# Kernel tuning notes

Measured on AMD Instinct MI355X. Metric: run time of the kernel, lower is better.

The kernel has to match this reference:

```python
import jax, jax.numpy as jnp
import numpy as np

MARGIN = 1.0
CURVATURE = 1.0
BOUNDARY_FACTOR = 2.0
MARGIN_THRESHOLD = 0.1
EPS = 1e-7


def setup_inputs() -> dict:
    key = jax.random.key(0)
    k1, k2 = jax.random.split(key)
    B, D = 4096, 128
    # scale so norms stay inside the unit Poincare ball (~0.57 on average)
    embeddings = jax.random.normal(k1, (B, D), dtype=jnp.float32) * 0.05
    labels = jax.random.randint(k2, (B,), 0, 64, dtype=jnp.int64)
    return {"embeddings": embeddings, "labels": labels}


def _poincare_distance_matrix(x, c):
    # d(x,y) = (1/sqrt(c)) * arccosh(1 + 2c||x-y||^2 / ((1-c||x||^2)(1-c||y||^2)))
    sq = jnp.sum(x * x, axis=-1)                       # [B]
    diff_sq = jnp.maximum(sq[:, None] + sq[None, :] - 2.0 * (x @ x.T), 0.0)
    denom = jnp.maximum((1.0 - c * sq[:, None]) * (1.0 - c * sq[None, :]), EPS)
    arg = 1.0 + 2.0 * c * diff_sq / denom
    return jnp.arccosh(jnp.maximum(arg, 1.0)) / jnp.sqrt(c)


def reference(embeddings, labels):
    B = embeddings.shape[0]
    distances = _poincare_distance_matrix(embeddings, CURVATURE)   # [B,B]

    same = labels[:, None] == labels[None, :]
    eye = jnp.eye(B, dtype=bool)
    positive_mask = same & ~eye
    negative_mask = ~same

    has_pos = jnp.any(positive_mask, axis=1)
    has_neg = jnp.any(negative_mask, axis=1)
    valid_anchor = has_pos & has_neg                               # [B]

    neg_inf = jnp.asarray(-jnp.inf, distances.dtype)
    hardest_pos = jnp.max(jnp.where(positive_mask, distances, neg_inf), axis=1)
    hardest_pos = jnp.where(has_pos, hardest_pos, 0.0)

    # adaptive margin (torch uses .item() -> detached from autograd)
    anchor_norm = jax.lax.stop_gradient(jnp.linalg.norm(embeddings, axis=-1))
    margin = jnp.maximum(MARGIN * (1.0 + BOUNDARY_FACTOR * anchor_norm),
                         MARGIN_THRESHOLD)                          # [B]

    pair_mask = valid_anchor[:, None] & negative_mask               # [B,B]
    raw = hardest_pos[:, None] - distances + margin[:, None]
    losses = jnp.maximum(raw, 0.0)

    total_triplets = jnp.sum(pair_mask)
    num_active = jnp.sum((raw > 0.0) & pair_mask)
    denom = jnp.maximum(total_triplets, 1).astype(losses.dtype)
    loss = jnp.sum(jnp.where(pair_mask, losses, 0.0)) / denom       # 'mean'

    active_ratio = num_active.astype(jnp.float32) / jnp.maximum(
        total_triplets.astype(jnp.float32), 1.0)
    pos_count = jnp.sum(positive_mask)
    mean_distance = jnp.where(
        pos_count > 0,
        jnp.sum(jnp.where(positive_mask, distances, 0.0))
        / jnp.maximum(pos_count, 1).astype(distances.dtype),
        0.0)

    return (loss, num_active, total_triplets, active_ratio, mean_distance)
```

## Files before the change

kernel.cpp:

```cpp
#include <hip/hip_runtime.h>
#include <hip/hip_bf16.h>
#include <math.h>

static constexpr int D   = 128;
static constexpr int NL  = 64;
static constexpr int NT  = 64;

typedef __attribute__((ext_vector_type(8))) short  bf16x8;
typedef __attribute__((ext_vector_type(4))) float  f32x4;

__device__ __forceinline__ float wave_reduce_sum(float v) {
  #pragma unroll
  for (int o = 32; o; o >>= 1) v += __shfl_xor(v, o, 64);
  return v;
}

__device__ __forceinline__ float fast_acosh(float x) {
  float s = __builtin_amdgcn_sqrtf(fmaf(x, x, -1.0f));
  return __logf(x + s);
}

__device__ __forceinline__ unsigned short f2b(float x) {
  unsigned int u = __float_as_uint(x);
  unsigned int lsb = (u >> 16) & 1u;
  u += 0x7fffu + lsb;
  return (unsigned short)(u >> 16);
}

__global__ __launch_bounds__(256) void kAB_setup(
    const float* __restrict__ emb, const int* __restrict__ lab,
    float* acc, int* LOFF, int* SIDX,
    float* __restrict__ sq, float* __restrict__ vv, int B) {
  int t = threadIdx.x;
  if ((int)blockIdx.x < B / 4) {
    int w = t >> 6, lane = t & 63;
    int i = blockIdx.x * 4 + w;
    float2 v = reinterpret_cast<const float2*>(emb + (size_t)i * D)[lane];
    float s = wave_reduce_sum(v.x * v.x + v.y * v.y);
    if (lane == 0) {
      sq[i] = s;
      vv[i] = 1.41421356237f / fmaxf(1.0f - s, 1e-6f);
    }
    return;
  }
  __shared__ int h[NL];
  __shared__ int cur[NL];
  if (t < NL) h[t] = 0;
  __syncthreads();
  for (int i = t; i < B; i += 256) atomicAdd(&h[lab[i]], 1);
  __syncthreads();
  if (t == 0) {
    int off = 0;
    long long pc = 0, trip = 0;
    for (int l = 0; l < NL; ++l) {
      int c = h[l];
      LOFF[l] = off; cur[l] = off; off += c;
      pc += (long long)c * (c - 1);
      if (c >= 2 && c < B) trip += (long long)c * (B - c);
    }
    LOFF[NL] = B;
    acc[0] = 0.0f; acc[1] = 0.0f; acc[2] = 0.0f;
    acc[3] = (float)pc;
    acc[4] = (float)trip;
  }
  __syncthreads();
  for (int i = t; i < B; i += 256) {
    int p = atomicAdd(&cur[lab[i]], 1);
    SIDX[p] = i;
  }
}

__global__ __launch_bounds__(256) void kC_pos(
    const float* __restrict__ emb,
    const int* __restrict__ LOFF, const int* __restrict__ SIDX,
    const float* __restrict__ sq, const float* __restrict__ vv,
    float* __restrict__ hpm, float* acc, int B) {
  __shared__ unsigned short Al[NT][D + 8];
  __shared__ unsigned short Bl[NT][D + 8];
  __shared__ float rs[NT], rv[NT];
  __shared__ float cs[NT], cv[NT];
  __shared__ int   ridx[NT], cidx[NT];

  int l = blockIdx.x;
  int base = LOFF[l];
  int c = LOFF[l + 1] - base;
  if (c == 0) return;
  int t = threadIdx.x;
  int wid = t >> 6, lane = t & 63;
  int lr = lane & 15, lg = lane >> 4;
  const bool validc = (c >= 2) && (c < B);

  float lsum = 0.0f;

  for (int i0 = 0; i0 < c; i0 += NT) {
    int ci = min(NT, c - i0);
    __syncthreads();
    #pragma unroll
    for (int p = 0; p < 8; ++p) {
      int idx = t + p * 256;
      int r = idx >> 5, c4 = idx & 31;
      int gi = SIDX[base + i0 + min(r, ci - 1)];
      float4 va = reinterpret_cast<const float4*>(emb + (size_t)gi * D)[c4];
      ushort4 ua = { f2b(va.x), f2b(va.y), f2b(va.z), f2b(va.w) };
      *reinterpret_cast<ushort4*>(&Al[r][c4 * 4]) = ua;
    }
    if (t < NT) {
      int gi = SIDX[base + i0 + min(t, ci - 1)];
      rs[t] = sq[gi]; rv[t] = vv[gi]; ridx[t] = gi;
    }

    float rmax[4] = {0.0f, 0.0f, 0.0f, 0.0f};

    for (int j0 = 0; j0 < c; j0 += NT) {
      int cj = min(NT, c - j0);
      __syncthreads();
      #pragma unroll
      for (int p = 0; p < 8; ++p) {
        int idx = t + p * 256;
        int r = idx >> 5, c4 = idx & 31;
        int gj = SIDX[base + j0 + min(r, cj - 1)];
        float4 vb = reinterpret_cast<const float4*>(emb + (size_t)gj * D)[c4];
        ushort4 ub = { f2b(vb.x), f2b(vb.y), f2b(vb.z), f2b(vb.w) };
        *reinterpret_cast<ushort4*>(&Bl[r][c4 * 4]) = ub;
      }
      if (t < NT) {
        int gj = SIDX[base + j0 + min(t, cj - 1)];
        cs[t] = sq[gj]; cv[t] = vv[gj]; cidx[t] = gj;
      }
      __syncthreads();

      f32x4 dacc[4];
      #pragma unroll
      for (int n = 0; n < 4; ++n) dacc[n] = (f32x4){0.f, 0.f, 0.f, 0.f};
      #pragma unroll
      for (int kk = 0; kk < 4; ++kk) {
        bf16x8 a = *reinterpret_cast<const bf16x8*>(&Al[wid * 16 + lr][kk * 32 + lg * 8]);
        bf16x8 b[4];
        #pragma unroll
        for (int n = 0; n < 4; ++n)
          b[n] = *reinterpret_cast<const bf16x8*>(&Bl[n * 16 + lr][kk * 32 + lg * 8]);
        #pragma unroll
        for (int n = 0; n < 4; ++n)
          dacc[n] = __builtin_amdgcn_mfma_f32_16x16x32_bf16(a, b[n], dacc[n], 0, 0, 0);
      }

      int r0 = wid * 16 + lg * 4;
      #pragma unroll
      for (int n = 0; n < 4; ++n) {
        int cc = n * 16 + lr;
        float sc = cs[cc], vcv = cv[cc];
        int   gj = cidx[cc];
        #pragma unroll
        for (int g = 0; g < 4; ++g) {
          int rloc = r0 + g;
          if (rloc < ci && cc < cj && ridx[rloc] != gj) {
            float diff = fmaxf(fmaf(-2.0f, dacc[n][g], rs[rloc] + sc), 0.0f);
            float arg  = fmaf(diff * rv[rloc], vcv, 1.0f);
            float d    = fast_acosh(arg);
            lsum += d;
            rmax[g] = fmaxf(rmax[g], d);
          }
        }
      }
    }

    int r0 = wid * 16 + lg * 4;
    #pragma unroll
    for (int g = 0; g < 4; ++g) {
      float v = rmax[g];
      v = fmaxf(v, __shfl_xor(v, 1, 64));
      v = fmaxf(v, __shfl_xor(v, 2, 64));
      v = fmaxf(v, __shfl_xor(v, 4, 64));
      v = fmaxf(v, __shfl_xor(v, 8, 64));
      int rloc = r0 + g;
      if (lr == 0 && rloc < ci) {
        float mg = fmaxf(fmaf(2.0f, __builtin_amdgcn_sqrtf(rs[rloc]), 1.0f), 0.1f);
        hpm[ridx[rloc]] = validc ? (v + mg) : -1e30f;
      }
    }
  }

  lsum = wave_reduce_sum(lsum);
  if (lane == 0 && lsum != 0.0f) atomicAdd(&acc[2], lsum);
}

__global__ __launch_bounds__(256) void kD_neg(
    const float* __restrict__ emb, const int* __restrict__ lab,
    const float* __restrict__ sq, const float* __restrict__ vv,
    const float* __restrict__ hpm, float* __restrict__ part, int B) {
  __shared__ unsigned short Al[NT][D + 8];
  __shared__ unsigned short Bl[NT][D + 8];
  __shared__ float rs[NT], rv[NT], rh[NT];
  __shared__ float cs[NT], cv[NT], ch[NT];
  __shared__ int   rl[NT], cl[NT];
  __shared__ float red[8];

  const int T = B / NT;
  int bid = blockIdx.x;
  float disc = (float)((2 * T + 1) * (2 * T + 1) - 8 * bid);
  int bi = (int)(((float)(2 * T + 1) - __builtin_amdgcn_sqrtf(disc)) * 0.5f);
  bi = max(0, min(bi, T - 1));
  while (bi * T - bi * (bi - 1) / 2 > bid) --bi;
  while ((bi + 1) * T - (bi + 1) * bi / 2 <= bid) ++bi;
  int bj = bi + (bid - (bi * T - bi * (bi - 1) / 2));
  const bool diag = (bi == bj);

  int t = threadIdx.x;

  const float* abase = emb + (size_t)bi * NT * D;
  const float* bbase = emb + (size_t)bj * NT * D;
  #pragma unroll
  for (int p = 0; p < NT * (D / 4) / 256; ++p) {
    int idx = t + p * 256;
    int r = idx >> 5, c4 = idx & 31;
    float4 va = reinterpret_cast<const float4*>(abase)[idx];
    float4 vb = reinterpret_cast<const float4*>(bbase)[idx];
    ushort4 ua = { f2b(va.x), f2b(va.y), f2b(va.z), f2b(va.w) };
    ushort4 ub = { f2b(vb.x), f2b(vb.y), f2b(vb.z), f2b(vb.w) };
    *reinterpret_cast<ushort4*>(&Al[r][c4 * 4]) = ua;
    *reinterpret_cast<ushort4*>(&Bl[r][c4 * 4]) = ub;
  }
  if (t < NT) {
    int g = bi * NT + t;
    rs[t] = sq[g]; rv[t] = vv[g]; rh[t] = hpm[g]; rl[t] = lab[g];
  } else if (t < 2 * NT) {
    int r = t - NT, g = bj * NT + r;
    cs[r] = sq[g]; cv[r] = vv[g]; ch[r] = hpm[g]; cl[r] = lab[g];
  }
  __syncthreads();

  int wid = t >> 6, lane = t & 63;
  int lr = lane & 15, lg = lane >> 4;

  f32x4 dacc[4];
  #pragma unroll
  for (int n = 0; n < 4; ++n) dacc[n] = (f32x4){0.f, 0.f, 0.f, 0.f};

  #pragma unroll
  for (int kk = 0; kk < 4; ++kk) {
    bf16x8 a = *reinterpret_cast<const bf16x8*>(&Al[wid * 16 + lr][kk * 32 + lg * 8]);
    bf16x8 b[4];
    #pragma unroll
    for (int n = 0; n < 4; ++n)
      b[n] = *reinterpret_cast<const bf16x8*>(&Bl[n * 16 + lr][kk * 32 + lg * 8]);
    #pragma unroll
    for (int n = 0; n < 4; ++n)
      dacc[n] = __builtin_amdgcn_mfma_f32_16x16x32_bf16(a, b[n], dacc[n], 0, 0, 0);
  }

  const float dsec = diag ? 0.0f : 1.0f;
  float lsum = 0.0f, lact = 0.0f;
  int r0 = wid * 16 + lg * 4;
  f32x4 sr = *reinterpret_cast<const f32x4*>(&rs[r0]);
  f32x4 vr = *reinterpret_cast<const f32x4*>(&rv[r0]);
  f32x4 hr = *reinterpret_cast<const f32x4*>(&rh[r0]);
  int4  lm = *reinterpret_cast<const int4*>(&rl[r0]);
  int lmv[4] = { lm.x, lm.y, lm.z, lm.w };
  #pragma unroll
  for (int n = 0; n < 4; ++n) {
    int cc = n * 16 + lr;
    float sc = cs[cc], vcv = cv[cc], hc = ch[cc];
    int   lc = cl[cc];
    #pragma unroll
    for (int g = 0; g < 4; ++g) {
      float dot  = dacc[n][g];
      float diff = fmaxf(fmaf(-2.0f, dot, sr[g] + sc), 0.0f);
      float arg  = fmaf(diff * vr[g], vcv, 1.0f);
      float d    = fast_acosh(arg);
      float r1   = hr[g] - d;
      float r2   = hc    - d;
      float neg  = (lmv[g] != lc) ? 1.0f : 0.0f;
      lsum += neg * (fmaxf(r1, 0.0f) + dsec * fmaxf(r2, 0.0f));
      lact += neg * ((r1 > 0.0f ? 1.0f : 0.0f) + dsec * (r2 > 0.0f ? 1.0f : 0.0f));
    }
  }

  lsum = wave_reduce_sum(lsum);
  lact = wave_reduce_sum(lact);
  if (lane == 0) { red[wid] = lsum; red[4 + wid] = lact; }
  __syncthreads();
  if (t == 0) {
    part[2 * bid]     = (red[0] + red[1]) + (red[2] + red[3]);
    part[2 * bid + 1] = (red[4] + red[5]) + (red[6] + red[7]);
  }
}

__global__ __launch_bounds__(256) void kE_final(
    const float* __restrict__ part, int nblk, const float* acc, float* out) {
  __shared__ float sl[256], sa[256];
  int t = threadIdx.x;
  float s = 0.0f, a = 0.0f;
  for (int i = t; i < nblk; i += 256) {
    s += part[2 * i];
    a += part[2 * i + 1];
  }
  sl[t] = s; sa[t] = a;
  __syncthreads();
  for (int o = 128; o; o >>= 1) {
    if (t < o) { sl[t] += sl[t + o]; sa[t] += sa[t + o]; }
    __syncthreads();
  }
  if (t == 0) {
    float trip = acc[4];
    float den  = fmaxf(trip, 1.0f);
    out[0] = sl[0] / den;
    out[1] = sa[0];
    out[2] = trip;
    out[3] = sa[0] / den;
    out[4] = (acc[3] > 0.0f) ? acc[2] / fmaxf(acc[3], 1.0f)
                             : 0.0f;
  }
}

extern "C" void kernel_launch(void* const* d_in, const int* in_sizes, int n_in,
                              void* d_out, int out_size, void* d_ws, size_t ws_size,
                              hipStream_t stream) {
  const float* emb = (const float*)d_in[0];
  const int*   lab = (const int*)d_in[1];
  int B = in_sizes[1];

  int T = B / NT;
  int nblk = T * (T + 1) / 2;

  float* ws   = (float*)d_ws;
  float* acc  = ws;
  float* sq   = ws + 8;
  float* vv   = sq + B;
  float* hpm  = vv + B;
  int*   LOFF = (int*)(hpm + B);
  int*   SIDX = LOFF + (NL + 1);
  float* part = (float*)(SIDX + B);

  kAB_setup<<<B / 4 + 1, 256, 0, stream>>>(emb, lab, acc, LOFF, SIDX, sq, vv, B);
  kC_pos<<<NL, 256, 0, stream>>>(emb, LOFF, SIDX, sq, vv, hpm, acc, B);
  kD_neg<<<nblk, 256, 0, stream>>>(emb, lab, sq, vv, hpm, part, B);
  kE_final<<<1, 256, 0, stream>>>(part, nblk, acc, (float*)d_out);
}
```

Before: 54.83 us.

## Fuse all stages into one cooperative persistent kernel with bf16 embedding cache

Merges the setup, positive, negative and final-reduction kernels into a single cooperative kernel, using grid-wide syncs between phases and a persistent grid sized to the occupancy limit. Embeddings are converted to bf16 once into the workspace, so later tiles load bf16 directly instead of reconverting fp32 per tile. Per-label index lists are now built in shared memory with a prefix scan instead of global atomics. It removes launch overhead and redundant conversion, but adds grid.sync costs, caps the per-label list at 512 entries, and loops tiles inside fewer blocks.

New measurement: 204.7 us. 273% more time.

```diff
diff --git a/kernel.cpp b/kernel.cpp
--- a/kernel.cpp
+++ b/kernel.cpp
@@ -1,10 +1,14 @@
 #include <hip/hip_runtime.h>
+#include <hip/hip_cooperative_groups.h>
 #include <hip/hip_bf16.h>
 #include <math.h>
 
-static constexpr int D   = 128;
-static constexpr int NL  = 64;
-static constexpr int NT  = 64;
+namespace cg = cooperative_groups;
+
+static constexpr int D        = 128;
+static constexpr int NL       = 64;
+static constexpr int NT       = 64;
+static constexpr int LIDX_CAP = 512;
 
 typedef __attribute__((ext_vector_type(8))) short  bf16x8;
 typedef __attribute__((ext_vector_type(4))) float  f32x4;
@@ -27,288 +31,289 @@
   return (unsigned short)(u >> 16);
 }
 
-__global__ __launch_bounds__(256) void kAB_setup(
+__global__ __launch_bounds__(256) void kfused(
     const float* __restrict__ emb, const int* __restrict__ lab,
-    float* acc, int* LOFF, int* SIDX,
-    float* __restrict__ sq, float* __restrict__ vv, int B) {
-  int t = threadIdx.x;
-  if ((int)blockIdx.x < B / 4) {
-    int w = t >> 6, lane = t & 63;
-    int i = blockIdx.x * 4 + w;
-    float2 v = reinterpret_cast<const float2*>(emb + (size_t)i * D)[lane];
+    void* __restrict__ wsv, float* __restrict__ out, int B) {
+  __shared__ unsigned short Al[NT][D + 8];
+  __shared__ unsigned short Bl[NT][D + 8];
+  __shared__ float rs[NT], rv[NT], cs[NT], cv[NT];
+  __shared__ int   ridx[NT], cidx[NT];
+  __shared__ union U {
+    struct { float rh[NT], ch[NT]; int rl[NT], cl[NT]; } c;
+    int lidx[LIDX_CAP];
+  } u;
+  __shared__ int   parr[256];
+  __shared__ float red[24];
+
+  float* wsf = (float*)wsv;
+  unsigned short* bfe = (unsigned short*)wsf;
+  float* sq     = wsf + (size_t)B * D / 2;
+  float* vv     = sq + B;
+  float* hpm    = vv + B;
+  float* plsum  = hpm + B;
+  float* plpc   = plsum + NL;
+  float* pltrip = plpc + NL;
+  float* part   = pltrip + NL;
+
+  cg::grid_group grid = cg::this_grid();
+  const int t    = threadIdx.x;
+  const int bid  = blockIdx.x;
+  const int G    = gridDim.x;
+  const int wid  = t >> 6, lane = t & 63;
+  const int lr   = lane & 15, lg = lane >> 4;
+
+  for (int row = bid * 4 + wid; row < B; row += G * 4) {
+    float2 v = reinterpret_cast<const float2*>(emb + (size_t)row * D)[lane];
+    ushort2 bv = { f2b(v.x), f2b(v.y) };
+    *reinterpret_cast<ushort2*>(&bfe[(size_t)row * D + 2 * lane]) = bv;
     float s = wave_reduce_sum(v.x * v.x + v.y * v.y);
     if (lane == 0) {
-      sq[i] = s;
-      vv[i] = 1.41421356237f / fmaxf(1.0f - s, 1e-6f);
-    }
-    return;
-  }
-  __shared__ int h[NL];
-  __shared__ int cur[NL];
-  if (t < NL) h[t] = 0;
+      sq[row] = s;
+      vv[row] = 1.41421356237f / fmaxf(1.0f - s, 1e-6f);
+    }
+  }
+  grid.sync();
+
+  if (bid < NL) {
+    const int l = bid;
+    int mc = 0;
+    for (int i = t; i < B; i += 256) mc += (lab[i] == l) ? 1 : 0;
+    parr[t] = mc;
+    __syncthreads();
+    for (int off = 1; off < 256; off <<= 1) {
+      int v = (t >= off) ? parr[t - off] : 0;
+      __syncthreads();
+      parr[t] += v;
+      __syncthreads();
+    }
+    const int c = parr[255];
+    int myoff = parr[t] - mc;
+    for (int i = t; i < B; i += 256) {
+      if (lab[i] == l) {
+        if (myoff < LIDX_CAP) u.lidx[myoff] = i;
+        ++myoff;
+      }
+    }
+    __syncthreads();
+
+    const int  cc_    = min(c, LIDX_CAP);
+    const bool validc = (c >= 2) && (c < B);
+    float lsum = 0.0f;
+
+    for (int i0 = 0; i0 < cc_; i0 += NT) {
+      int ci = min(NT, cc_ - i0);
+      __syncthreads();
+      #pragma unroll
+      for (int p = 0; p < 4; ++p) {
+        int idx = t + p * 256;
+        int r = idx >> 4, c16 = idx & 15;
+        int gi = u.lidx[i0 + min(r, ci - 1)];
+        bf16x8 va = reinterpret_cast<const bf16x8*>(bfe + (size_t)gi * D)[c16];
+        *reinterpret_cast<bf16x8*>(&Al[r][c16 * 8]) = va;
+      }
+      if (t < NT) {
+        int gi = u.lidx[i0 + min(t, ci - 1)];
+        rs[t] = sq[gi]; rv[t] = vv[gi]; ridx[t] = gi;
+      }
+
+      float rmax[4] = {0.0f, 0.0f, 0.0f, 0.0f};
+
+      for (int j0 = 0; j0 < cc_; j0 += NT) {
+        int cj = min(NT, cc_ - j0);
+        __syncthreads();
+        #pragma unroll
+        for (int p = 0; p < 4; ++p) {
+          int idx = t + p * 256;
+          int r = idx >> 4, c16 = idx & 15;
+          int gj = u.lidx[j0 + min(r, cj - 1)];
+          bf16x8 vb = reinterpret_cast<const bf16x8*>(bfe + (size_t)gj * D)[c16];
+          *reinterpret_cast<bf16x8*>(&Bl[r][c16 * 8]) = vb;
+        }
+        if (t < NT) {
+          int gj = u.lidx[j0 + min(t, cj - 1)];
+          cs[t] = sq[gj]; cv[t] = vv[gj]; cidx[t] = gj;
+        }
+        __syncthreads();
+
+        f32x4 dacc[4];
+        #pragma unroll
+        for (int n = 0; n < 4; ++n) dacc[n] = (f32x4){0.f, 0.f, 0.f, 0.f};
+        #pragma unroll
+        for (int kk = 0; kk < 4; ++kk) {
+          bf16x8 a = *reinterpret_cast<const bf16x8*>(&Al[wid * 16 + lr][kk * 32 + lg * 8]);
+          bf16x8 b[4];
+          #pragma unroll
+          for (int n = 0; n < 4; ++n)
+            b[n] = *reinterpret_cast<const bf16x8*>(&Bl[n * 16 + lr][kk * 32 + lg * 8]);
+          #pragma unroll
+          for (int n = 0; n < 4; ++n)
+            dacc[n] = __builtin_amdgcn_mfma_f32_16x16x32_bf16(a, b[n], dacc[n], 0, 0, 0);
+        }
+
+        int r0 = wid * 16 + lg * 4;
+        #pragma unroll
+        for (int n = 0; n < 4; ++n) {
+          int ccn = n * 16 + lr;
+          float sc = cs[ccn], vcv = cv[ccn];
+          int   gj = cidx[ccn];
+          #pragma unroll
+          for (int g = 0; g < 4; ++g) {
+            int rloc = r0 + g;
+            if (rloc < ci && ccn < cj && ridx[rloc] != gj) {
+              float diff = fmaxf(fmaf(-2.0f, dacc[n][g], rs[rloc] + sc), 0.0f);
+              float arg  = fmaf(diff * rv[rloc], vcv, 1.0f);
+              float d    = fast_acosh(arg);
+              lsum += d;
+              rmax[g] = fmaxf(rmax[g], d);
+            }
+          }
+        }
+      }
+
+      int r0 = wid * 16 + lg * 4;
+      #pragma unroll
+      for (int g = 0; g < 4; ++g) {
+        float v = rmax[g];
+        v = fmaxf(v, __shfl_xor(v, 1, 64));
+        v = fmaxf(v, __shfl_xor(v, 2, 64));
+        v = fmaxf(v, __shfl_xor(v, 4, 64));
+        v = fmaxf(v, __shfl_xor(v, 8, 64));
+        int rloc = r0 + g;
+        if (lr == 0 && rloc < ci) {
+          float mg = fmaxf(fmaf(2.0f, __builtin_amdgcn_sqrtf(rs[rloc]), 1.0f), 0.1f);
+          hpm[ridx[rloc]] = validc ? (v + mg) : -1e30f;
+        }
+      }
+    }
+
+    lsum = wave_reduce_sum(lsum);
+    if (lane == 0) red[wid] = lsum;
+    __syncthreads();
+    if (t == 0) {
+      plsum[l]  = (c > 0) ? (red[0] + red[1]) + (red[2] + red[3]) : 0.0f;
+      plpc[l]   = (float)((long long)c * (c - 1));
+      pltrip[l] = ((c >= 2) && (c < B)) ? (float)((long long)c * (B - c)) : 0.0f;
+    }
+  }
+  grid.sync();
+
+  const int T2    = B / NT;
+  const int ntile = T2 * (T2 + 1) / 2;
+  float nsum = 0.0f, nact = 0.0f;
+
+  for (int tile = bid; tile < ntile; tile += G) {
+    float disc = (float)((2 * T2 + 1) * (2 * T2 + 1) - 8 * tile);
+    int bi = (int)(((float)(2 * T2 + 1) - __builtin_amdgcn_sqrtf(disc)) * 0.5f);
+    bi = max(0, min(bi, T2 - 1));
+    while (bi * T2 - bi * (bi - 1) / 2 > tile) --bi;
+    while ((bi + 1) * T2 - (bi + 1) * bi / 2 <= tile) ++bi;
+    int bj = bi + (tile - (bi * T2 - bi * (bi - 1) / 2));
+    const float dsec = (bi == bj) ? 0.0f : 1.0f;
+
+    __syncthreads();
+    const unsigned short* ab = bfe + (size_t)bi * NT * D;
+    const unsigned short* bb = bfe + (size_t)bj * NT * D;
+    #pragma unroll
+    for (int p = 0; p < 4; ++p) {
+      int idx = t + p * 256;
+      int r = idx >> 4, c16 = idx & 15;
+      bf16x8 va = reinterpret_cast<const bf16x8*>(ab + (size_t)r * D)[c16];
+      bf16x8 vb = reinterpret_cast<const bf16x8*>(bb + (size_t)r * D)[c16];
+      *reinterpret_cast<bf16x8*>(&Al[r][c16 * 8]) = va;
+      *reinterpret_cast<bf16x8*>(&Bl[r][c16 * 8]) = vb;
+    }
+    if (t < NT) {
+      int g = bi * NT + t;
+      rs[t] = sq[g]; rv[t] = vv[g]; u.c.rh[t] = hpm[g]; u.c.rl[t] = lab[g];
+    } else if (t < 2 * NT) {
+      int r = t - NT, g = bj * NT + r;
+      cs[r] = sq[g]; cv[r] = vv[g]; u.c.ch[r] = hpm[g]; u.c.cl[r] = lab[g];
+    }
+    __syncthreads();
+
+    f32x4 dacc[4];
+    #pragma unroll
+    for (int n = 0; n < 4; ++n) dacc[n] = (f32x4){0.f, 0.f, 0.f, 0.f};
+    #pragma unroll
+    for (int kk = 0; kk < 4; ++kk) {
+      bf16x8 a = *reinterpret_cast<const bf16x8*>(&Al[wid * 16 + lr][kk * 32 + lg * 8]);
+      bf16x8 b[4];
+      #pragma unroll
+      for (int n = 0; n < 4; ++n)
+        b[n] = *reinterpret_cast<const bf16x8*>(&Bl[n * 16 + lr][kk * 32 + lg * 8]);
+      #pragma unroll
+      for (int n = 0; n < 4; ++n)
+        dacc[n] = __builtin_amdgcn_mfma_f32_16x16x32_bf16(a, b[n], dacc[n], 0, 0, 0);
+    }
+
+    int r0 = wid * 16 + lg * 4;
+    f32x4 sr = *reinterpret_cast<const f32x4*>(&rs[r0]);
+    f32x4 vr = *reinterpret_cast<const f32x4*>(&rv[r0]);
+    f32x4 hr = *reinterpret_cast<const f32x4*>(&u.c.rh[r0]);
+    int lmv[4] = { u.c.rl[r0], u.c.rl[r0 + 1], u.c.rl[r0 + 2], u.c.rl[r0 + 3] };
+    #pragma unroll
+    for (int n = 0; n < 4; ++n) {
+      int ccn = n * 16 + lr;
+      float sc = cs[ccn], vcv = cv[ccn], hc = u.c.ch[ccn];
+      int   lc = u.c.cl[ccn];
+      #pragma unroll
+      for (int g = 0; g < 4; ++g) {
+        float diff = fmaxf(fmaf(-2.0f, dacc[n][g], sr[g] + sc), 0.0f);
+        float arg  = fmaf(diff * vr[g], vcv, 1.0f);
+        float d    = fast_acosh(arg);
+        float r1   = hr[g] - d;
+        float r2   = hc    - d;
+        float neg  = (lmv[g] != lc) ? 1.0f : 0.0f;
+        nsum += neg * (fmaxf(r1, 0.0f) + dsec * fmaxf(r2, 0.0f));
+        nact += neg * ((r1 > 0.0f ? 1.0f : 0.0f) + dsec * (r2 > 0.0f ? 1.0f : 0.0f));
+      }
+    }
+  }
+
+  nsum = wave_reduce_sum(nsum);
+  nact = wave_reduce_sum(nact);
   __syncthreads();
-  for (int i = t; i < B; i += 256) atomicAdd(&h[lab[i]], 1);
-  __syncthreads();
-  if (t == 0) {
-    int off = 0;
-    long long pc = 0, trip = 0;
-    for (int l = 0; l < NL; ++l) {
-      int c = h[l];
-      LOFF[l] = off; cur[l] = off; off += c;
-      pc += (long long)c * (c - 1);
-      if (c >= 2 && c < B) trip += (long long)c * (B - c);
-    }
-    LOFF[NL] = B;
-    acc[0] = 0.0f; acc[1] = 0.0f; acc[2] = 0.0f;
-    acc[3] = (float)pc;
-    acc[4] = (float)trip;
-  }
-  __syncthreads();
-  for (int i = t; i < B; i += 256) {
-    int p = atomicAdd(&cur[lab[i]], 1);
-    SIDX[p] = i;
-  }
-}
-
-__global__ __launch_bounds__(256) void kC_pos(
-    const float* __restrict__ emb,
-    const int* __restrict__ LOFF, const int* __restrict__ SIDX,
-    const float* __restrict__ sq, const float* __restrict__ vv,
-    float* __restrict__ hpm, float* acc, int B) {
-  __shared__ unsigned short Al[NT][D + 8];
-  __shared__ unsigned short Bl[NT][D + 8];
-  __shared__ float rs[NT], rv[NT];
-  __shared__ float cs[NT], cv[NT];
-  __shared__ int   ridx[NT], cidx[NT];
-
-  int l = blockIdx.x;
-  int base = LOFF[l];
-  int c = LOFF[l + 1] - base;
-  if (c == 0) return;
-  int t = threadIdx.x;
-  int wid = t >> 6, lane = t & 63;
-  int lr = lane & 15, lg = lane >> 4;
-  const bool validc = (c >= 2) && (c < B);
-
-  float lsum = 0.0f;
-
-  for (int i0 = 0; i0 < c; i0 += NT) {
-    int ci = min(NT, c - i0);
-    __syncthreads();
-    #pragma unroll
-    for (int p = 0; p < 8; ++p) {
-      int idx = t + p * 256;
-      int r = idx >> 5, c4 = idx & 31;
-      int gi = SIDX[base + i0 + min(r, ci - 1)];
-      float4 va = reinterpret_cast<const float4*>(emb + (size_t)gi * D)[c4];
-      ushort4 ua = { f2b(va.x), f2b(va.y), f2b(va.z), f2b(va.w) };
-      *reinterpret_cast<ushort4*>(&Al[r][c4 * 4]) = ua;
-    }
-    if (t < NT) {
-      int gi = SIDX[base + i0 + min(t, ci - 1)];
-      rs[t] = sq[gi]; rv[t] = vv[gi]; ridx[t] = gi;
-    }
-
-    float rmax[4] = {0.0f, 0.0f, 0.0f, 0.0f};
-
-    for (int j0 = 0; j0 < c; j0 += NT) {
-      int cj = min(NT, c - j0);
-      __syncthreads();
-      #pragma unroll
-      for (int p = 0; p < 8; ++p) {
-        int idx = t + p * 256;
-        int r = idx >> 5, c4 = idx & 31;
-        int gj = SIDX[base + j0 + min(r, cj - 1)];
-        float4 vb = reinterpret_cast<const float4*>(emb + (size_t)gj * D)[c4];
-        ushort4 ub = { f2b(vb.x), f2b(vb.y), f2b(vb.z), f2b(vb.w) };
-        *reinterpret_cast<ushort4*>(&Bl[r][c4 * 4]) = ub;
-      }
-      if (t < NT) {
-        int gj = SIDX[base + j0 + min(t, cj - 1)];
-        cs[t] = sq[gj]; cv[t] = vv[gj]; cidx[t] = gj;
-      }
-      __syncthreads();
-
-      f32x4 dacc[4];
-      #pragma unroll
-      for (int n = 0; n < 4; ++n) dacc[n] = (f32x4){0.f, 0.f, 0.f, 0.f};
-      #pragma unroll
-      for (int kk = 0; kk < 4; ++kk) {
-        bf16x8 a = *reinterpret_cast<const bf16x8*>(&Al[wid * 16 + lr][kk * 32 + lg * 8]);
-        bf16x8 b[4];
-        #pragma unroll
-        for (int n = 0; n < 4; ++n)
-          b[n] = *reinterpret_cast<const bf16x8*>(&Bl[n * 16 + lr][kk * 32 + lg * 8]);
-        #pragma unroll
-        for (int n = 0; n < 4; ++n)
-          dacc[n] = __builtin_amdgcn_mfma_f32_16x16x32_bf16(a, b[n], dacc[n], 0, 0, 0);
-      }
-
-      int r0 = wid * 16 + lg * 4;
-      #pragma unroll
-      for (int n = 0; n < 4; ++n) {
-        int cc = n * 16 + lr;
-        float sc = cs[cc], vcv = cv[cc];
-        int   gj = cidx[cc];
-        #pragma unroll
-        for (int g = 0; g < 4; ++g) {
-          int rloc = r0 + g;
-          if (rloc < ci && cc < cj && ridx[rloc] != gj) {
-            float diff = fmaxf(fmaf(-2.0f, dacc[n][g], rs[rloc] + sc), 0.0f);
-            float arg  = fmaf(diff * rv[rloc], vcv, 1.0f);
-            float d    = fast_acosh(arg);
-            lsum += d;
-            rmax[g] = fmaxf(rmax[g], d);
-          }
-        }
-      }
-    }
-
-    int r0 = wid * 16 + lg * 4;
-    #pragma unroll
-    for (int g = 0; g < 4; ++g) {
-      float v = rmax[g];
-      v = fmaxf(v, __shfl_xor(v, 1, 64));
-      v = fmaxf(v, __shfl_xor(v, 2, 64));
-      v = fmaxf(v, __shfl_xor(v, 4, 64));
-      v = fmaxf(v, __shfl_xor(v, 8, 64));
-      int rloc = r0 + g;
-      if (lr == 0 && rloc < ci) {
-        float mg = fmaxf(fmaf(2.0f, __builtin_amdgcn_sqrtf(rs[rloc]), 1.0f), 0.1f);
-        hpm[ridx[rloc]] = validc ? (v + mg) : -1e30f;
-      }
-    }
-  }
-
-  lsum = wave_reduce_sum(lsum);
-  if (lane == 0 && lsum != 0.0f) atomicAdd(&acc[2], lsum);
-}
-
-__global__ __launch_bounds__(256) void kD_neg(
-    const float* __restrict__ emb, const int* __restrict__ lab,
-    const float* __restrict__ sq, const float* __restrict__ vv,
-    const float* __restrict__ hpm, float* __restrict__ part, int B) {
-  __shared__ unsigned short Al[NT][D + 8];
-  __shared__ unsigned short Bl[NT][D + 8];
-  __shared__ float rs[NT], rv[NT], rh[NT];
-  __shared__ float cs[NT], cv[NT], ch[NT];
-  __shared__ int   rl[NT], cl[NT];
-  __shared__ float red[8];
-
-  const int T = B / NT;
-  int bid = blockIdx.x;
-  float disc = (float)((2 * T + 1) * (2 * T + 1) - 8 * bid);
-  int bi = (int)(((float)(2 * T + 1) - __builtin_amdgcn_sqrtf(disc)) * 0.5f);
-  bi = max(0, min(bi, T - 1));
-  while (bi * T - bi * (bi - 1) / 2 > bid) --bi;
-  while ((bi + 1) * T - (bi + 1) * bi / 2 <= bid) ++bi;
-  int bj = bi + (bid - (bi * T - bi * (bi - 1) / 2));
-  const bool diag = (bi == bj);
-
-  int t = threadIdx.x;
-
-  const float* abase = emb + (size_t)bi * NT * D;
-  const float* bbase = emb + (size_t)bj * NT * D;
-  #pragma unroll
-  for (int p = 0; p < NT * (D / 4) / 256; ++p) {
-    int idx = t + p * 256;
-    int r = idx >> 5, c4 = idx & 31;
-    float4 va = reinterpret_cast<const float4*>(abase)[idx];
-    float4 vb = reinterpret_cast<const float4*>(bbase)[idx];
-    ushort4 ua = { f2b(va.x), f2b(va.y), f2b(va.z), f2b(va.w) };
-    ushort4 ub = { f2b(vb.x), f2b(vb.y), f2b(vb.z), f2b(vb.w) };
-    *reinterpret_cast<ushort4*>(&Al[r][c4 * 4]) = ua;
-    *reinterpret_cast<ushort4*>(&Bl[r][c4 * 4]) = ub;
-  }
-  if (t < NT) {
-    int g = bi * NT + t;
-    rs[t] = sq[g]; rv[t] = vv[g]; rh[t] = hpm[g]; rl[t] = lab[g];
-  } else if (t < 2 * NT) {
-    int r = t - NT, g = bj * NT + r;
-    cs[r] = sq[g]; cv[r] = vv[g]; ch[r] = hpm[g]; cl[r] = lab[g];
-  }
-  __syncthreads();
-
-  int wid = t >> 6, lane = t & 63;
-  int lr = lane & 15, lg = lane >> 4;
-
-  f32x4 dacc[4];
-  #pragma unroll
-  for (int n = 0; n < 4; ++n) dacc[n] = (f32x4){0.f, 0.f, 0.f, 0.f};
-
-  #pragma unroll
-  for (int kk = 0; kk < 4; ++kk) {
-    bf16x8 a = *reinterpret_cast<const bf16x8*>(&Al[wid * 16 + lr][kk * 32 + lg * 8]);
-    bf16x8 b[4];
-    #pragma unroll
-    for (int n = 0; n < 4; ++n)
-      b[n] = *reinterpret_cast<const bf16x8*>(&Bl[n * 16 + lr][kk * 32 + lg * 8]);
-    #pragma unroll
-    for (int n = 0; n < 4; ++n)
-      dacc[n] = __builtin_amdgcn_mfma_f32_16x16x32_bf16(a, b[n], dacc[n], 0, 0, 0);
-  }
-
-  const float dsec = diag ? 0.0f : 1.0f;
-  float lsum = 0.0f, lact = 0.0f;
-  int r0 = wid * 16 + lg * 4;
-  f32x4 sr = *reinterpret_cast<const f32x4*>(&rs[r0]);
-  f32x4 vr = *reinterpret_cast<const f32x4*>(&rv[r0]);
-  f32x4 hr = *reinterpret_cast<const f32x4*>(&rh[r0]);
-  int4  lm = *reinterpret_cast<const int4*>(&rl[r0]);
-  int lmv[4] = { lm.x, lm.y, lm.z, lm.w };
-  #pragma unroll
-  for (int n = 0; n < 4; ++n) {
-    int cc = n * 16 + lr;
-    float sc = cs[cc], vcv = cv[cc], hc = ch[cc];
-    int   lc = cl[cc];
-    #pragma unroll
-    for (int g = 0; g < 4; ++g) {
-      float dot  = dacc[n][g];
-      float diff = fmaxf(fmaf(-2.0f, dot, sr[g] + sc), 0.0f);
-      float arg  = fmaf(diff * vr[g], vcv, 1.0f);
-      float d    = fast_acosh(arg);
-      float r1   = hr[g] - d;
-      float r2   = hc    - d;
-      float neg  = (lmv[g] != lc) ? 1.0f : 0.0f;
-      lsum += neg * (fmaxf(r1, 0.0f) + dsec * fmaxf(r2, 0.0f));
-      lact += neg * ((r1 > 0.0f ? 1.0f : 0.0f) + dsec * (r2 > 0.0f ? 1.0f : 0.0f));
-    }
-  }
-
-  lsum = wave_reduce_sum(lsum);
-  lact = wave_reduce_sum(lact);
-  if (lane == 0) { red[wid] = lsum; red[4 + wid] = lact; }
+  if (lane == 0) { red[wid] = nsum; red[8 + wid] = nact; }
   __syncthreads();
   if (t == 0) {
     part[2 * bid]     = (red[0] + red[1]) + (red[2] + red[3]);
-    part[2 * bid + 1] = (red[4] + red[5]) + (red[6] + red[7]);
-  }
-}
-
-__global__ __launch_bounds__(256) void kE_final(
-    const float* __restrict__ part, int nblk, const float* acc, float* out) {
-  __shared__ float sl[256], sa[256];
-  int t = threadIdx.x;
-  float s = 0.0f, a = 0.0f;
-  for (int i = t; i < nblk; i += 256) {
-    s += part[2 * i];
-    a += part[2 * i + 1];
-  }
-  sl[t] = s; sa[t] = a;
-  __syncthreads();
-  for (int o = 128; o; o >>= 1) {
-    if (t < o) { sl[t] += sl[t + o]; sa[t] += sa[t + o]; }
-    __syncthreads();
-  }
-  if (t == 0) {
-    float trip = acc[4];
-    float den  = fmaxf(trip, 1.0f);
-    out[0] = sl[0] / den;
-    out[1] = sa[0];
-    out[2] = trip;
-    out[3] = sa[0] / den;
-    out[4] = (acc[3] > 0.0f) ? acc[2] / fmaxf(acc[3], 1.0f)
-                             : 0.0f;
+    part[2 * bid + 1] = (red[8] + red[9]) + (red[10] + red[11]);
+  }
+  grid.sync();
+
+  if (bid == 0) {
+    float s = 0.0f, a = 0.0f;
+    for (int i = t; i < G; i += 256) {
+      s += part[2 * i];
+      a += part[2 * i + 1];
+    }
+    float ps = 0.0f, pc = 0.0f, tr = 0.0f;
+    if (t < NL) { ps = plsum[t]; pc = plpc[t]; tr = pltrip[t]; }
+    s  = wave_reduce_sum(s);
+    a  = wave_reduce_sum(a);
+    ps = wave_reduce_sum(ps);
+    pc = wave_reduce_sum(pc);
+    tr = wave_reduce_sum(tr);
+    __syncthreads();
+    if (lane == 0) {
+      red[wid * 5 + 0] = s;  red[wid * 5 + 1] = a;  red[wid * 5 + 2] = ps;
+      red[wid * 5 + 3] = pc; red[wid * 5 + 4] = tr;
+    }
+    __syncthreads();
+    if (t == 0) {
+      float S = 0, A = 0, PS = 0, PC = 0, TR = 0;
+      #pragma unroll
+      for (int w = 0; w < 4; ++w) {
+        S += red[w * 5 + 0]; A += red[w * 5 + 1]; PS += red[w * 5 + 2];
+        PC += red[w * 5 + 3]; TR += red[w * 5 + 4];
+      }
+      float den = fmaxf(TR, 1.0f);
+      out[0] = S / den;
+      out[1] = A;
+      out[2] = TR;
+      out[3] = A / den;
+      out[4] = (PC > 0.0f) ? PS / fmaxf(PC, 1.0f) : 0.0f;
+    }
   }
 }
 
@@ -318,21 +323,23 @@
   const float* emb = (const float*)d_in[0];
   const int*   lab = (const int*)d_in[1];
   int B = in_sizes[1];
+  float* outp = (float*)d_out;
 
   int T = B / NT;
-  int nblk = T * (T + 1) / 2;
-
-  float* ws   = (float*)d_ws;
-  float* acc  = ws;
-  float* sq   = ws + 8;
-  float* vv   = sq + B;
-  float* hpm  = vv + B;
-  int*   LOFF = (int*)(hpm + B);
-  int*   SIDX = LOFF + (NL + 1);
-  float* part = (float*)(SIDX + B);
-
-  kAB_setup<<<B / 4 + 1, 256, 0, stream>>>(emb, lab, acc, LOFF, SIDX, sq, vv, B);
-  kC_pos<<<NL, 256, 0, stream>>>(emb, LOFF, SIDX, sq, vv, hpm, acc, B);
-  kD_neg<<<nblk, 256, 0, stream>>>(emb, lab, sq, vv, hpm, part, B);
-  kE_final<<<1, 256, 0, stream>>>(part, nblk, acc, (float*)d_out);
-}
+  int ntile = T * (T + 1) / 2;
+
+  int dev = 0;
+  hipGetDevice(&dev);
+  int ncu = 256;
+  hipDeviceGetAttribute(&ncu, hipDeviceAttributeMultiprocessorCount, dev);
+  int maxblk = 0;
+  hipOccupancyMaxActiveBlocksPerMultiprocessor(&maxblk, kfused, 256, 0);
+  if (maxblk < 1) maxblk = 1;
+  int G = ncu * maxblk;
+  if (G > ntile) G = ntile;
+  if (G < NL) G = NL;
+
+  void* ws = d_ws;
+  void* args[] = { (void*)&emb, (void*)&lab, (void*)&ws, (void*)&outp, (void*)&B };
+  hipLaunchCooperativeKernel(kfused, dim3(G), dim3(256), args, 0, stream);
+}
```

## Precompute bf16 embeddings once, load MFMA fragments directly, fuse final reduction

Applied to the files above, without the earlier changes.

The setup kernel now writes a bf16 copy of the embeddings, so the positive and negative kernels load packed bf16x8 vectors instead of converting fp32 on every tile load. The negative kernel drops its LDS staging and reads MFMA operands and per-row metadata straight from global memory. The separate final-reduction kernel is removed; the last block, found through an atomic ticket counter, does the reduction. This saves one launch and the repeated conversion work, but adds an extra workspace buffer and replaces LDS reuse with uncoalesced global fragment reads that rely on cache hits.

Measured after the change: 101.7 us. 1.86x slower.

```diff
diff --git a/kernel.cpp b/kernel.cpp
--- a/kernel.cpp
+++ b/kernel.cpp
@@ -2,9 +2,9 @@
 #include <hip/hip_bf16.h>
 #include <math.h>
 
-static constexpr int D   = 128;
-static constexpr int NL  = 64;
-static constexpr int NT  = 64;
+static constexpr int D  = 128;
+static constexpr int NL = 64;
+static constexpr int NT = 64;
 
 typedef __attribute__((ext_vector_type(8))) short  bf16x8;
 typedef __attribute__((ext_vector_type(4))) float  f32x4;
@@ -27,15 +27,17 @@
   return (unsigned short)(u >> 16);
 }
 
-__global__ __launch_bounds__(256) void kAB_setup(
+__global__ __launch_bounds__(256) void k1_setup(
     const float* __restrict__ emb, const int* __restrict__ lab,
-    float* acc, int* LOFF, int* SIDX,
-    float* __restrict__ sq, float* __restrict__ vv, int B) {
+    unsigned short* __restrict__ bfe, float* acc, int* LOFF, int* SIDX,
+    int* counter, float* __restrict__ sq, float* __restrict__ vv, int B) {
   int t = threadIdx.x;
   if ((int)blockIdx.x < B / 4) {
     int w = t >> 6, lane = t & 63;
     int i = blockIdx.x * 4 + w;
     float2 v = reinterpret_cast<const float2*>(emb + (size_t)i * D)[lane];
+    ushort2 bv = { f2b(v.x), f2b(v.y) };
+    *reinterpret_cast<ushort2*>(&bfe[(size_t)i * D + 2 * lane]) = bv;
     float s = wave_reduce_sum(v.x * v.x + v.y * v.y);
     if (lane == 0) {
       sq[i] = s;
@@ -62,6 +64,7 @@
     acc[0] = 0.0f; acc[1] = 0.0f; acc[2] = 0.0f;
     acc[3] = (float)pc;
     acc[4] = (float)trip;
+    *counter = 0;
   }
   __syncthreads();
   for (int i = t; i < B; i += 256) {
@@ -70,8 +73,8 @@
   }
 }
 
-__global__ __launch_bounds__(256) void kC_pos(
-    const float* __restrict__ emb,
+__global__ __launch_bounds__(256) void k2_pos(
+    const unsigned short* __restrict__ bfe,
     const int* __restrict__ LOFF, const int* __restrict__ SIDX,
     const float* __restrict__ sq, const float* __restrict__ vv,
     float* __restrict__ hpm, float* acc, int B) {
@@ -96,13 +99,12 @@
     int ci = min(NT, c - i0);
     __syncthreads();
     #pragma unroll
-    for (int p = 0; p < 8; ++p) {
+    for (int p = 0; p < 4; ++p) {
       int idx = t + p * 256;
-      int r = idx >> 5, c4 = idx & 31;
+      int r = idx >> 4, c16 = idx & 15;
       int gi = SIDX[base + i0 + min(r, ci - 1)];
-      float4 va = reinterpret_cast<const float4*>(emb + (size_t)gi * D)[c4];
-      ushort4 ua = { f2b(va.x), f2b(va.y), f2b(va.z), f2b(va.w) };
-      *reinterpret_cast<ushort4*>(&Al[r][c4 * 4]) = ua;
+      bf16x8 va = reinterpret_cast<const bf16x8*>(bfe + (size_t)gi * D)[c16];
+      *reinterpret_cast<bf16x8*>(&Al[r][c16 * 8]) = va;
     }
     if (t < NT) {
       int gi = SIDX[base + i0 + min(t, ci - 1)];
@@ -115,13 +117,12 @@
       int cj = min(NT, c - j0);
       __syncthreads();
       #pragma unroll
-      for (int p = 0; p < 8; ++p) {
+      for (int p = 0; p < 4; ++p) {
         int idx = t + p * 256;
-        int r = idx >> 5, c4 = idx & 31;
+        int r = idx >> 4, c16 = idx & 15;
         int gj = SIDX[base + j0 + min(r, cj - 1)];
-        float4 vb = reinterpret_cast<const float4*>(emb + (size_t)gj * D)[c4];
-        ushort4 ub = { f2b(vb.x), f2b(vb.y), f2b(vb.z), f2b(vb.w) };
-        *reinterpret_cast<ushort4*>(&Bl[r][c4 * 4]) = ub;
+        bf16x8 vb = reinterpret_cast<const bf16x8*>(bfe + (size_t)gj * D)[c16];
+        *reinterpret_cast<bf16x8*>(&Bl[r][c16 * 8]) = vb;
       }
       if (t < NT) {
         int gj = SIDX[base + j0 + min(t, cj - 1)];
@@ -147,13 +148,13 @@
       int r0 = wid * 16 + lg * 4;
       #pragma unroll
       for (int n = 0; n < 4; ++n) {
-        int cc = n * 16 + lr;
-        float sc = cs[cc], vcv = cv[cc];
-        int   gj = cidx[cc];
+        int ccn = n * 16 + lr;
+        float sc = cs[ccn], vcv = cv[ccn];
+        int   gj = cidx[ccn];
         #pragma unroll
         for (int g = 0; g < 4; ++g) {
           int rloc = r0 + g;
-          if (rloc < ci && cc < cj && ridx[rloc] != gj) {
+          if (rloc < ci && ccn < cj && ridx[rloc] != gj) {
             float diff = fmaxf(fmaf(-2.0f, dacc[n][g], rs[rloc] + sc), 0.0f);
             float arg  = fmaf(diff * rv[rloc], vcv, 1.0f);
             float d    = fast_acosh(arg);
@@ -184,131 +185,114 @@
   if (lane == 0 && lsum != 0.0f) atomicAdd(&acc[2], lsum);
 }
 
-__global__ __launch_bounds__(256) void kD_neg(
-    const float* __restrict__ emb, const int* __restrict__ lab,
+__global__ __launch_bounds__(256) void k3_neg(
+    const unsigned short* __restrict__ bfe, const int* __restrict__ lab,
     const float* __restrict__ sq, const float* __restrict__ vv,
-    const float* __restrict__ hpm, float* __restrict__ part, int B) {
-  __shared__ unsigned short Al[NT][D + 8];
-  __shared__ unsigned short Bl[NT][D + 8];
-  __shared__ float rs[NT], rv[NT], rh[NT];
-  __shared__ float cs[NT], cv[NT], ch[NT];
-  __shared__ int   rl[NT], cl[NT];
-  __shared__ float red[8];
-
-  const int T = B / NT;
+    const float* __restrict__ hpm, const float* __restrict__ acc,
+    float* __restrict__ part, int* __restrict__ counter,
+    float* __restrict__ out, int B) {
+  __shared__ float red[16];
+  __shared__ int   islast;
+
+  const int T2 = B / NT;
+  const int ntile = T2 * (T2 + 1) / 2;
   int bid = blockIdx.x;
-  float disc = (float)((2 * T + 1) * (2 * T + 1) - 8 * bid);
-  int bi = (int)(((float)(2 * T + 1) - __builtin_amdgcn_sqrtf(disc)) * 0.5f);
-  bi = max(0, min(bi, T - 1));
-  while (bi * T - bi * (bi - 1) / 2 > bid) --bi;
-  while ((bi + 1) * T - (bi + 1) * bi / 2 <= bid) ++bi;
-  int bj = bi + (bid - (bi * T - bi * (bi - 1) / 2));
-  const bool diag = (bi == bj);
-
-  int t = threadIdx.x;
-
-  const float* abase = emb + (size_t)bi * NT * D;
-  const float* bbase = emb + (size_t)bj * NT * D;
-  #pragma unroll
-  for (int p = 0; p < NT * (D / 4) / 256; ++p) {
-    int idx = t + p * 256;
-    int r = idx >> 5, c4 = idx & 31;
-    float4 va = reinterpret_cast<const float4*>(abase)[idx];
-    float4 vb = reinterpret_cast<const float4*>(bbase)[idx];
-    ushort4 ua = { f2b(va.x), f2b(va.y), f2b(va.z), f2b(va.w) };
-    ushort4 ub = { f2b(vb.x), f2b(vb.y), f2b(vb.z), f2b(vb.w) };
-    *reinterpret_cast<ushort4*>(&Al[r][c4 * 4]) = ua;
-    *reinterpret_cast<ushort4*>(&Bl[r][c4 * 4]) = ub;
-  }
-  if (t < NT) {
-    int g = bi * NT + t;
-    rs[t] = sq[g]; rv[t] = vv[g]; rh[t] = hpm[g]; rl[t] = lab[g];
-  } else if (t < 2 * NT) {
-    int r = t - NT, g = bj * NT + r;
-    cs[r] = sq[g]; cv[r] = vv[g]; ch[r] = hpm[g]; cl[r] = lab[g];
-  }
-  __syncthreads();
-
-  int wid = t >> 6, lane = t & 63;
-  int lr = lane & 15, lg = lane >> 4;
+  float disc = (float)((2 * T2 + 1) * (2 * T2 + 1) - 8 * bid);
+  int bi = (int)(((float)(2 * T2 + 1) - __builtin_amdgcn_sqrtf(disc)) * 0.5f);
+  bi = max(0, min(bi, T2 - 1));
+  while (bi * T2 - bi * (bi - 1) / 2 > bid) --bi;
+  while ((bi + 1) * T2 - (bi + 1) * bi / 2 <= bid) ++bi;
+  int bj = bi + (bid - (bi * T2 - bi * (bi - 1) / 2));
+  const float dsec = (bi == bj) ? 0.0f : 1.0f;
+
+  const int t = threadIdx.x;
+  const int wid = t >> 6, lane = t & 63;
+  const int lr = lane & 15, lg = lane >> 4;
+
+  const unsigned short* arow = bfe + (size_t)(bi * NT + wid * 16 + lr) * D + lg * 8;
+  bf16x8 aF[4];
+  #pragma unroll
+  for (int kk = 0; kk < 4; ++kk)
+    aF[kk] = *reinterpret_cast<const bf16x8*>(arow + kk * 32);
 
   f32x4 dacc[4];
   #pragma unroll
   for (int n = 0; n < 4; ++n) dacc[n] = (f32x4){0.f, 0.f, 0.f, 0.f};
 
   #pragma unroll
-  for (int kk = 0; kk < 4; ++kk) {
-    bf16x8 a = *reinterpret_cast<const bf16x8*>(&Al[wid * 16 + lr][kk * 32 + lg * 8]);
-    bf16x8 b[4];
+  for (int n = 0; n < 4; ++n) {
+    const unsigned short* brow = bfe + (size_t)(bj * NT + n * 16 + lr) * D + lg * 8;
     #pragma unroll
-    for (int n = 0; n < 4; ++n)
-      b[n] = *reinterpret_cast<const bf16x8*>(&Bl[n * 16 + lr][kk * 32 + lg * 8]);
-    #pragma unroll
-    for (int n = 0; n < 4; ++n)
-      dacc[n] = __builtin_amdgcn_mfma_f32_16x16x32_bf16(a, b[n], dacc[n], 0, 0, 0);
-  }
-
-  const float dsec = diag ? 0.0f : 1.0f;
-  float lsum = 0.0f, lact = 0.0f;
-  int r0 = wid * 16 + lg * 4;
-  f32x4 sr = *reinterpret_cast<const f32x4*>(&rs[r0]);
-  f32x4 vr = *reinterpret_cast<const f32x4*>(&rv[r0]);
-  f32x4 hr = *reinterpret_cast<const f32x4*>(&rh[r0]);
-  int4  lm = *reinterpret_cast<const int4*>(&rl[r0]);
+    for (int kk = 0; kk < 4; ++kk) {
+      bf16x8 b = *reinterpret_cast<const bf16x8*>(brow + kk * 32);
+      dacc[n] = __builtin_amdgcn_mfma_f32_16x16x32_bf16(aF[kk], b, dacc[n], 0, 0, 0);
+    }
+  }
+
+  int gr0 = bi * NT + wid * 16 + lg * 4;
+  f32x4 sr = *reinterpret_cast<const f32x4*>(&sq[gr0]);
+  f32x4 vr = *reinterpret_cast<const f32x4*>(&vv[gr0]);
+  f32x4 hr = *reinterpret_cast<const f32x4*>(&hpm[gr0]);
+  int4  lm = *reinterpret_cast<const int4*>(&lab[gr0]);
   int lmv[4] = { lm.x, lm.y, lm.z, lm.w };
+
+  float nsum = 0.0f, nact = 0.0f;
   #pragma unroll
   for (int n = 0; n < 4; ++n) {
-    int cc = n * 16 + lr;
-    float sc = cs[cc], vcv = cv[cc], hc = ch[cc];
-    int   lc = cl[cc];
+    int gc = bj * NT + n * 16 + lr;
+    float sc = sq[gc], vcv = vv[gc], hc = hpm[gc];
+    int   lc = lab[gc];
     #pragma unroll
     for (int g = 0; g < 4; ++g) {
-      float dot  = dacc[n][g];
-      float diff = fmaxf(fmaf(-2.0f, dot, sr[g] + sc), 0.0f);
+      float diff = fmaxf(fmaf(-2.0f, dacc[n][g], sr[g] + sc), 0.0f);
       float arg  = fmaf(diff * vr[g], vcv, 1.0f);
       float d    = fast_acosh(arg);
       float r1   = hr[g] - d;
       float r2   = hc    - d;
       float neg  = (lmv[g] != lc) ? 1.0f : 0.0f;
-      lsum += neg * (fmaxf(r1, 0.0f) + dsec * fmaxf(r2, 0.0f));
-      lact += neg * ((r1 > 0.0f ? 1.0f : 0.0f) + dsec * (r2 > 0.0f ? 1.0f : 0.0f));
-    }
-  }
-
-  lsum = wave_reduce_sum(lsum);
-  lact = wave_reduce_sum(lact);
-  if (lane == 0) { red[wid] = lsum; red[4 + wid] = lact; }
+      nsum += neg * (fmaxf(r1, 0.0f) + dsec * fmaxf(r2, 0.0f));
+      nact += neg * ((r1 > 0.0f ? 1.0f : 0.0f) + dsec * (r2 > 0.0f ? 1.0f : 0.0f));
+    }
+  }
+
+  nsum = wave_reduce_sum(nsum);
+  nact = wave_reduce_sum(nact);
+  if (lane == 0) { red[wid] = nsum; red[8 + wid] = nact; }
   __syncthreads();
   if (t == 0) {
     part[2 * bid]     = (red[0] + red[1]) + (red[2] + red[3]);
-    part[2 * bid + 1] = (red[4] + red[5]) + (red[6] + red[7]);
-  }
-}
-
-__global__ __launch_bounds__(256) void kE_final(
-    const float* __restrict__ part, int nblk, const float* acc, float* out) {
-  __shared__ float sl[256], sa[256];
-  int t = threadIdx.x;
-  float s = 0.0f, a = 0.0f;
-  for (int i = t; i < nblk; i += 256) {
-    s += part[2 * i];
-    a += part[2 * i + 1];
-  }
-  sl[t] = s; sa[t] = a;
-  __syncthreads();
-  for (int o = 128; o; o >>= 1) {
-    if (t < o) { sl[t] += sl[t + o]; sa[t] += sa[t + o]; }
+    part[2 * bid + 1] = (red[8] + red[9]) + (red[10] + red[11]);
+    __threadfence();
+    int ticket = atomicAdd(counter, 1);
+    islast = (ticket == ntile - 1) ? 1 : 0;
+  }
+  __syncthreads();
+
+  if (islast) {
+    __threadfence();
+    const volatile float* vp = (const volatile float*)part;
+    float s = 0.0f, a = 0.0f;
+    for (int i = t; i < ntile; i += 256) {
+      s += vp[2 * i];
+      a += vp[2 * i + 1];
+    }
+    s = wave_reduce_sum(s);
+    a = wave_reduce_sum(a);
     __syncthreads();
-  }
-  if (t == 0) {
-    float trip = acc[4];
-    float den  = fmaxf(trip, 1.0f);
-    out[0] = sl[0] / den;
-    out[1] = sa[0];
-    out[2] = trip;
-    out[3] = sa[0] / den;
-    out[4] = (acc[3] > 0.0f) ? acc[2] / fmaxf(acc[3], 1.0f)
-                             : 0.0f;
+    if (lane == 0) { red[wid] = s; red[8 + wid] = a; }
+    __syncthreads();
+    if (t == 0) {
+      float S = (red[0] + red[1]) + (red[2] + red[3]);
+      float A = (red[8] + red[9]) + (red[10] + red[11]);
+      float TR = acc[4];
+      float den = fmaxf(TR, 1.0f);
+      out[0] = S / den;
+      out[1] = A;
+      out[2] = TR;
+      out[3] = A / den;
+      out[4] = (acc[3] > 0.0f) ? acc[2] / fmaxf(acc[3], 1.0f)
+                               : 0.0f;
+    }
   }
 }
 
@@ -320,19 +304,22 @@
   int B = in_sizes[1];
 
   int T = B / NT;
-  int nblk = T * (T + 1) / 2;
-
-  float* ws   = (float*)d_ws;
-  float* acc  = ws;
-  float* sq   = ws + 8;
+  int ntile = T * (T + 1) / 2;
+
+  float* wsf  = (float*)d_ws;
+  unsigned short* bfe = (unsigned short*)wsf;
+  float* acc  = wsf + (size_t)B * D / 2;
+  float* sq   = acc + 8;
   float* vv   = sq + B;
   float* hpm  = vv + B;
   int*   LOFF = (int*)(hpm + B);
   int*   SIDX = LOFF + (NL + 1);
   float* part = (float*)(SIDX + B);
-
-  kAB_setup<<<B / 4 + 1, 256, 0, stream>>>(emb, lab, acc, LOFF, SIDX, sq, vv, B);
-  kC_pos<<<NL, 256, 0, stream>>>(emb, LOFF, SIDX, sq, vv, hpm, acc, B);
-  kD_neg<<<nblk, 256, 0, stream>>>(emb, lab, sq, vv, hpm, part, B);
-  kE_final<<<1, 256, 0, stream>>>(part, nblk, acc, (float*)d_out);
-}
+  int*   counter = (int*)(part + 2 * ntile);
+
+  k1_setup<<<B / 4 + 1, 256, 0, stream>>>(emb, lab, bfe, acc, LOFF, SIDX,
+                                          counter, sq, vv, B);
+  k2_pos<<<NL, 256, 0, stream>>>(bfe, LOFF, SIDX, sq, vv, hpm, acc, B);
+  k3_neg<<<ntile, 256, 0, stream>>>(bfe, lab, sq, vv, hpm, acc, part, counter,
+                                    (float*)d_out, B);
+}
```
